# Optimization experiments

Measured on AMD Instinct MI355X. Metric: run time of the kernel, lower is better.

## Reference

```python
import jax, jax.numpy as jnp
import numpy as np

N_NODES = 8192
F_IN = 4
H1, H2 = 32, 16


def setup_inputs() -> dict:
    key = jax.random.key(0)
    ks = jax.random.split(key, 5)
    x = jax.random.normal(ks[0], (N_NODES, F_IN), dtype=jnp.float32)
    src = jnp.arange(N_NODES - 1, dtype=jnp.int32)
    edge_index = jnp.stack([src, src + 1])  # [2, N-1] directed chain i -> i+1
    W1 = jax.random.normal(ks[1], (F_IN, H1), dtype=jnp.float32) * (1.0 / np.sqrt(F_IN))
    W2 = jax.random.normal(ks[2], (H1, H2), dtype=jnp.float32) * (1.0 / np.sqrt(H1))
    W3 = jax.random.normal(ks[3], (H2, N_NODES), dtype=jnp.float32) * (1.0 / np.sqrt(H2))
    b1 = jnp.zeros((H1,), jnp.float32)
    b2 = jnp.zeros((H2,), jnp.float32)
    b3 = jnp.zeros((N_NODES,), jnp.float32)
    return {"x": x, "W1": W1, "b1": b1, "W2": W2, "b2": b2,
            "W3": W3, "b3": b3, "edge_index": edge_index}


def reference(x, W1, b1, W2, b2, W3, b3, edge_index):
    n = x.shape[0]
    row, col = edge_index[0], edge_index[1]
    # GCNConv: add self-loops, symmetric normalization deg^{-1/2} A_hat deg^{-1/2}
    loops = jnp.arange(n, dtype=row.dtype)
    row = jnp.concatenate([row, loops])
    col = jnp.concatenate([col, loops])
    deg = jax.ops.segment_sum(jnp.ones(row.shape, x.dtype), col, num_segments=n)
    dis = jnp.where(deg > 0, jax.lax.rsqrt(jnp.maximum(deg, 1e-12)), 0.0)
    norm = dis[row] * dis[col]  # [E + N]

    def gcn_conv(h, W, b):
        h = h @ W                               # transform first (PyG order)
        msg = norm[:, None] * h[row]            # gather + scale
        out = jax.ops.segment_sum(msg, col, num_segments=n)  # scatter-add
        return out + b

    h = jax.nn.relu(gcn_conv(x, W1, b1))
    h = jax.nn.relu(gcn_conv(h, W2, b2))
    return gcn_conv(h, W3, b3)
```

## Files before the change

### kernel.cpp

```cpp
#include <hip/hip_runtime.h>


#define N_NODES 8192
#define F_IN 4
#define H1 32
#define H2 16

#define COLS_PER_BLOCK 1024
#define ROWS_PER_BLOCK 32

__device__ __forceinline__ float coefA(int j) { return j == 0 ? 1.0f : 0.5f; }
__device__ __forceinline__ float coefC(int j) {
    return j <= 0 ? 0.0f : (j == 1 ? 0.70710678118654752f : 0.5f);
}

__global__ void __launch_bounds__(256) gnn_fused(
    const float* __restrict__ x,  const float* __restrict__ W1,
    const float* __restrict__ b1, const float* __restrict__ W2,
    const float* __restrict__ b2, const float* __restrict__ W3,
    const float* __restrict__ b3, float* __restrict__ out)
{
    __shared__ float sW1t[H1 * F_IN];
    __shared__ float sb1[H1];
    __shared__ float sW2[H1 * H2];
    __shared__ float sb2[H2];
    __shared__ float st2[ROWS_PER_BLOCK + 2][H2];
    __shared__ float gs[ROWS_PER_BLOCK][H2];

    const int t = threadIdx.x;
    const int row0 = blockIdx.y * ROWS_PER_BLOCK;

    if (t < H1 * F_IN) sW1t[t] = W1[(t & 3) * H1 + (t >> 2)];
    if (t < H1) sb1[t] = b1[t];
    if (t < H2) sb2[t] = b2[t];
    sW2[t] = W2[t];
    sW2[t + 256] = W2[t + 256];
    __syncthreads();

    if (t < ROWS_PER_BLOCK + 2) {
        const int jj = row0 - 2 + t;
        float acc[H2];
        #pragma unroll
        for (int m = 0; m < H2; ++m) acc[m] = 0.f;
        if (jj >= 0) {
            const float4 xc = *reinterpret_cast<const float4*>(&x[jj * F_IN]);
            float4 xp = make_float4(0.f, 0.f, 0.f, 0.f);
            if (jj >= 1) xp = *reinterpret_cast<const float4*>(&x[(jj - 1) * F_IN]);
            const float a = coefA(jj), c = coefC(jj);
            #pragma unroll
            for (int k = 0; k < H1; ++k) {
                const float4 wk = *reinterpret_cast<const float4*>(&sW1t[k * 4]);
                const float t1c = xc.x * wk.x + xc.y * wk.y + xc.z * wk.z + xc.w * wk.w;
                const float t1p = xp.x * wk.x + xp.y * wk.y + xp.z * wk.z + xp.w * wk.w;
                float h = a * t1c + c * t1p + sb1[k];
                h = h > 0.f ? h : 0.f;
                #pragma unroll
                for (int m = 0; m < H2; ++m) acc[m] += h * sW2[k * H2 + m];
            }
        }
        #pragma unroll
        for (int m = 0; m < H2; ++m) st2[t][m] = acc[m];
    }
    __syncthreads();

    if (t < ROWS_PER_BLOCK) {
        const int j = row0 + t;
        const float aj = coefA(j),     cj = coefC(j);
        const float ap = coefA(j - 1), cp = coefC(j - 1);
        #pragma unroll
        for (int m = 0; m < H2; ++m) {
            const float bm = sb2[m];
            float h2c = aj * st2[t + 2][m] + cj * st2[t + 1][m] + bm;
            h2c = h2c > 0.f ? h2c : 0.f;
            float h2p = ap * st2[t + 1][m] + cp * st2[t][m] + bm;
            h2p = h2p > 0.f ? h2p : 0.f;
            gs[t][m] = aj * h2c + cj * h2p;
        }
    }
    __syncthreads();

    const int col0 = blockIdx.x * COLS_PER_BLOCK + t * 4;
    float4 w[H2];
    #pragma unroll
    for (int k = 0; k < H2; ++k)
        w[k] = *reinterpret_cast<const float4*>(&W3[k * N_NODES + col0]);
    const float4 bb = *reinterpret_cast<const float4*>(&b3[col0]);

    float* po = out + (size_t)row0 * N_NODES + col0;
    #pragma unroll 4
    for (int r = 0; r < ROWS_PER_BLOCK; ++r) {
        float4 acc = bb;
        #pragma unroll
        for (int k = 0; k < H2; ++k) {
            const float gv = gs[r][k];
            acc.x += gv * w[k].x;
            acc.y += gv * w[k].y;
            acc.z += gv * w[k].z;
            acc.w += gv * w[k].w;
        }
        *reinterpret_cast<float4*>(po) = acc;
        po += N_NODES;
    }
}

extern "C" void kernel_launch(void* const* d_in, const int* in_sizes, int n_in,
                              void* d_out, int out_size, void* d_ws, size_t ws_size,
                              hipStream_t stream) {
    const float* x  = (const float*)d_in[0];
    const float* W1 = (const float*)d_in[1];
    const float* b1 = (const float*)d_in[2];
    const float* W2 = (const float*)d_in[3];
    const float* b2 = (const float*)d_in[4];
    const float* W3 = (const float*)d_in[5];
    const float* b3 = (const float*)d_in[6];

    float* out = (float*)d_out;

    dim3 grid(N_NODES / COLS_PER_BLOCK, N_NODES / ROWS_PER_BLOCK);
    gnn_fused<<<grid, 256, 0, stream>>>(x, W1, b1, W2, b2, W3, b3, out);
}
```

Baseline: 59.38 us.

## Split fused kernel into front hidden-state kernel and output GEMM kernel

Moves the layer-1/2 computation into a separate kernel that writes the 8192x16 hidden matrix to workspace once, instead of every output block redundantly recomputing it for its rows across all 8 column blocks. The output kernel then reads rows of g from global memory (broadcast loads, cached) and does the rank-16 product. It adds a second launch and a global round-trip for g, and removes the barriers and serial front work from the output-bound kernel.

```diff
diff --git a/kernel.cpp b/kernel.cpp
--- a/kernel.cpp
+++ b/kernel.cpp
@@ -6,6 +6,7 @@
 #define H1 32
 #define H2 16
 
+#define FRONT_ROWS 128
 #define COLS_PER_BLOCK 1024
 #define ROWS_PER_BLOCK 32
 
@@ -14,21 +15,19 @@
     return j <= 0 ? 0.0f : (j == 1 ? 0.70710678118654752f : 0.5f);
 }
 
-__global__ void __launch_bounds__(256) gnn_fused(
+__global__ void __launch_bounds__(256) gnn_front(
     const float* __restrict__ x,  const float* __restrict__ W1,
     const float* __restrict__ b1, const float* __restrict__ W2,
-    const float* __restrict__ b2, const float* __restrict__ W3,
-    const float* __restrict__ b3, float* __restrict__ out)
+    const float* __restrict__ b2, float* __restrict__ g)
 {
     __shared__ float sW1t[H1 * F_IN];
     __shared__ float sb1[H1];
     __shared__ float sW2[H1 * H2];
     __shared__ float sb2[H2];
-    __shared__ float st2[ROWS_PER_BLOCK + 2][H2];
-    __shared__ float gs[ROWS_PER_BLOCK][H2];
+    __shared__ float st2[FRONT_ROWS + 2][H2];
 
     const int t = threadIdx.x;
-    const int row0 = blockIdx.y * ROWS_PER_BLOCK;
+    const int row0 = blockIdx.x * FRONT_ROWS;
 
     if (t < H1 * F_IN) sW1t[t] = W1[(t & 3) * H1 + (t >> 2)];
     if (t < H1) sb1[t] = b1[t];
@@ -37,7 +36,7 @@
     sW2[t + 256] = W2[t + 256];
     __syncthreads();
 
-    if (t < ROWS_PER_BLOCK + 2) {
+    if (t < FRONT_ROWS + 2) {
         const int jj = row0 - 2 + t;
         float acc[H2];
         #pragma unroll
@@ -63,10 +62,11 @@
     }
     __syncthreads();
 
-    if (t < ROWS_PER_BLOCK) {
+    if (t < FRONT_ROWS) {
         const int j = row0 + t;
         const float aj = coefA(j),     cj = coefC(j);
         const float ap = coefA(j - 1), cp = coefC(j - 1);
+        float gout[H2];
         #pragma unroll
         for (int m = 0; m < H2; ++m) {
             const float bm = sb2[m];
@@ -74,30 +74,56 @@
             h2c = h2c > 0.f ? h2c : 0.f;
             float h2p = ap * st2[t + 1][m] + cp * st2[t][m] + bm;
             h2p = h2p > 0.f ? h2p : 0.f;
-            gs[t][m] = aj * h2c + cj * h2p;
+            gout[m] = aj * h2c + cj * h2p;
+        }
+        #pragma unroll
+        for (int m = 0; m < H2; m += 4) {
+            *reinterpret_cast<float4*>(&g[j * H2 + m]) =
+                make_float4(gout[m], gout[m + 1], gout[m + 2], gout[m + 3]);
         }
     }
-    __syncthreads();
+}
 
+__global__ void __launch_bounds__(256) gnn_out(
+    const float* __restrict__ g, const float* __restrict__ W3,
+    const float* __restrict__ b3, float* __restrict__ out)
+{
+    const int t = threadIdx.x;
     const int col0 = blockIdx.x * COLS_PER_BLOCK + t * 4;
+    const int row0 = blockIdx.y * ROWS_PER_BLOCK;
+
     float4 w[H2];
     #pragma unroll
     for (int k = 0; k < H2; ++k)
         w[k] = *reinterpret_cast<const float4*>(&W3[k * N_NODES + col0]);
     const float4 bb = *reinterpret_cast<const float4*>(&b3[col0]);
 
+    const float* gr = g + row0 * H2;
     float* po = out + (size_t)row0 * N_NODES + col0;
+
     #pragma unroll 4
     for (int r = 0; r < ROWS_PER_BLOCK; ++r) {
+        const float4 g0 = *reinterpret_cast<const float4*>(&gr[r * H2 + 0]);
+        const float4 g1 = *reinterpret_cast<const float4*>(&gr[r * H2 + 4]);
+        const float4 g2 = *reinterpret_cast<const float4*>(&gr[r * H2 + 8]);
+        const float4 g3 = *reinterpret_cast<const float4*>(&gr[r * H2 + 12]);
         float4 acc = bb;
-        #pragma unroll
-        for (int k = 0; k < H2; ++k) {
-            const float gv = gs[r][k];
-            acc.x += gv * w[k].x;
-            acc.y += gv * w[k].y;
-            acc.z += gv * w[k].z;
-            acc.w += gv * w[k].w;
-        }
+        acc.x += g0.x*w[0].x;  acc.y += g0.x*w[0].y;  acc.z += g0.x*w[0].z;  acc.w += g0.x*w[0].w;
+        acc.x += g0.y*w[1].x;  acc.y += g0.y*w[1].y;  acc.z += g0.y*w[1].z;  acc.w += g0.y*w[1].w;
+        acc.x += g0.z*w[2].x;  acc.y += g0.z*w[2].y;  acc.z += g0.z*w[2].z;  acc.w += g0.z*w[2].w;
+        acc.x += g0.w*w[3].x;  acc.y += g0.w*w[3].y;  acc.z += g0.w*w[3].z;  acc.w += g0.w*w[3].w;
+        acc.x += g1.x*w[4].x;  acc.y += g1.x*w[4].y;  acc.z += g1.x*w[4].z;  acc.w += g1.x*w[4].w;
+        acc.x += g1.y*w[5].x;  acc.y += g1.y*w[5].y;  acc.z += g1.y*w[5].z;  acc.w += g1.y*w[5].w;
+        acc.x += g1.z*w[6].x;  acc.y += g1.z*w[6].y;  acc.z += g1.z*w[6].z;  acc.w += g1.z*w[6].w;
+        acc.x += g1.w*w[7].x;  acc.y += g1.w*w[7].y;  acc.z += g1.w*w[7].z;  acc.w += g1.w*w[7].w;
+        acc.x += g2.x*w[8].x;  acc.y += g2.x*w[8].y;  acc.z += g2.x*w[8].z;  acc.w += g2.x*w[8].w;
+        acc.x += g2.y*w[9].x;  acc.y += g2.y*w[9].y;  acc.z += g2.y*w[9].z;  acc.w += g2.y*w[9].w;
+        acc.x += g2.z*w[10].x; acc.y += g2.z*w[10].y; acc.z += g2.z*w[10].z; acc.w += g2.z*w[10].w;
+        acc.x += g2.w*w[11].x; acc.y += g2.w*w[11].y; acc.z += g2.w*w[11].z; acc.w += g2.w*w[11].w;
+        acc.x += g3.x*w[12].x; acc.y += g3.x*w[12].y; acc.z += g3.x*w[12].z; acc.w += g3.x*w[12].w;
+        acc.x += g3.y*w[13].x; acc.y += g3.y*w[13].y; acc.z += g3.y*w[13].z; acc.w += g3.y*w[13].w;
+        acc.x += g3.z*w[14].x; acc.y += g3.z*w[14].y; acc.z += g3.z*w[14].z; acc.w += g3.z*w[14].w;
+        acc.x += g3.w*w[15].x; acc.y += g3.w*w[15].y; acc.z += g3.w*w[15].z; acc.w += g3.w*w[15].w;
         *reinterpret_cast<float4*>(po) = acc;
         po += N_NODES;
     }
@@ -114,8 +140,11 @@
     const float* W3 = (const float*)d_in[5];
     const float* b3 = (const float*)d_in[6];
 
+    float* g   = (float*)d_ws;
     float* out = (float*)d_out;
 
+    gnn_front<<<N_NODES / FRONT_ROWS, 256, 0, stream>>>(x, W1, b1, W2, b2, g);
+
     dim3 grid(N_NODES / COLS_PER_BLOCK, N_NODES / ROWS_PER_BLOCK);
-    gnn_fused<<<grid, 256, 0, stream>>>(x, W1, b1, W2, b2, W3, b3, out);
+    gnn_out<<<grid, 256, 0, stream>>>(g, W3, b3, out);
 }
```

Result: faster. 54.41 us (-8.4%).
